# Optimization experiments

Measured on AMD Instinct MI355X. Metric: run time of the kernel, lower is better.

The kernel has to match this reference:

```python
import jax, jax.numpy as jnp
import numpy as np

N_WIRES = 4
N_LAYERS = 3
DIM = 2 ** N_WIRES  # 16-element statevector


def _ry(t):
    # RY(t) = [[cos(t/2), -sin(t/2)], [sin(t/2), cos(t/2)]]
    c, s = jnp.cos(t * 0.5), jnp.sin(t * 0.5)
    return jnp.stack([jnp.stack([c, -s], -1), jnp.stack([s, c], -1)], -2).astype(jnp.complex64)


def _rz(t):
    # RZ(t) = diag(e^{-it/2}, e^{+it/2})
    e = jnp.exp(-0.5j * t.astype(jnp.complex64))
    z = jnp.zeros_like(e)
    return jnp.stack([jnp.stack([e, z], -1), jnp.stack([z, jnp.conj(e)], -1)], -2)


def _rx(t):
    # RX(t) = [[cos(t/2), -i sin(t/2)], [-i sin(t/2), cos(t/2)]]
    c = jnp.cos(t * 0.5).astype(jnp.complex64)
    s = (-1j) * jnp.sin(t * 0.5).astype(jnp.complex64)
    return jnp.stack([jnp.stack([c, s], -1), jnp.stack([s, c], -1)], -2)


def _apply_1q(state, U, q):
    # state: (B, 16) complex; U: (B,2,2) batched or (2,2) shared; wire 0 = most significant
    B = state.shape[0]
    left, right = 2 ** q, 2 ** (N_WIRES - 1 - q)
    s = state.reshape(B, left, 2, right)
    if U.ndim == 3:
        s = jnp.einsum('bij,bajc->baic', U, s)
    else:
        s = jnp.einsum('ij,bajc->baic', U, s)
    return s.reshape(B, DIM)


def _apply_cnot(state, c):
    # CNOT with control wire c, target wire c+1 (adjacent)
    B = state.shape[0]
    left, right = 2 ** c, 2 ** (N_WIRES - 2 - c)
    s = state.reshape(B, left, 2, 2, right)
    s = s.at[:, :, 1].set(s[:, :, 1, ::-1])
    return s.reshape(B, DIM)


def setup_inputs() -> dict:
    key = jax.random.key(0)
    k1, k2 = jax.random.split(key)
    B = 524288
    x = jax.random.normal(k1, (B, N_WIRES), dtype=jnp.float32)
    params = jax.random.normal(k2, (N_LAYERS, N_WIRES, 3), dtype=jnp.float32) * 0.1
    return {'x': x, 'params': params}


def reference(x, params):
    B = x.shape[0]
    state = jnp.zeros((B, DIM), jnp.complex64).at[:, 0].set(1.0)
    # RYZXY encoding (batched gates)
    for i in range(N_WIRES):
        state = _apply_1q(state, _ry(x[:, i]), i)
        state = _apply_1q(state, _rz(x[:, (i + 1) % N_WIRES]), i)
        state = _apply_1q(state, _rx(x[:, (i + 2) % N_WIRES]), i)
        state = _apply_1q(state, _ry(x[:, (i + 3) % N_WIRES]), i)
    # variational layers: Rot(phi,theta,omega) = RZ(omega) @ RY(theta) @ RZ(phi), then CNOT chain
    for l in range(N_LAYERS):
        for q in range(N_WIRES):
            phi, th, om = params[l, q, 0], params[l, q, 1], params[l, q, 2]
            U = _rz(om) @ _ry(th) @ _rz(phi)
            state = _apply_1q(state, U, q)
        for q in range(N_WIRES - 1):
            state = _apply_cnot(state, q)
    # Pauli-Z expectation on each wire
    probs = (state.real ** 2 + state.imag ** 2).reshape((B,) + (2,) * N_WIRES)
    sign = jnp.array([1.0, -1.0], jnp.float32)
    outs = []
    for q in range(N_WIRES):
        shp = [1] * (N_WIRES + 1)
        shp[q + 1] = 2
        outs.append(jnp.sum(probs * sign.reshape(shp), axis=tuple(range(1, N_WIRES + 1))))
    return jnp.stack(outs, axis=1)  # (B, n_wires)
```

## Files before the change

### kernel.cpp

```cpp
#include <hip/hip_runtime.h>

#define N_WIRES 4
#define N_LAYERS 3
#define DIM 16

__device__ __forceinline__ float2 cmul(float2 a, float2 b) {
    return make_float2(a.x * b.x - a.y * b.y, a.x * b.y + a.y * b.x);
}
__device__ __forceinline__ float2 cadd(float2 a, float2 b) {
    return make_float2(a.x + b.x, a.y + b.y);
}

__global__ __launch_bounds__(256) void qenc_kernel(
    const float4* __restrict__ x4, const float* __restrict__ params,
    float4* __restrict__ out4, int B)
{
    __shared__ __align__(16) float Us[N_LAYERS * N_WIRES][8];
    const int t = threadIdx.x;
    if (t < N_LAYERS * N_WIRES) {
        const float phi = params[t * 3 + 0];
        const float th  = params[t * 3 + 1];
        const float om  = params[t * 3 + 2];
        float c, s, ca, sa, cb, sb;
        __sincosf(0.5f * th, &s, &c);
        __sincosf(0.5f * (phi + om), &sa, &ca);
        __sincosf(0.5f * (phi - om), &sb, &cb);
        Us[t][0] =  c * ca;  Us[t][1] = -c * sa;
        Us[t][2] = -s * cb;  Us[t][3] = -s * sb;
        Us[t][4] =  s * cb;  Us[t][5] = -s * sb;
        Us[t][6] =  c * ca;  Us[t][7] =  c * sa;
    }
    __syncthreads();

    const int b = blockIdx.x * blockDim.x + t;
    if (b >= B) return;

    const float4 xv = x4[b];
    const float xa[4] = {xv.x, xv.y, xv.z, xv.w};
    float cx[4], sx[4];
#pragma unroll
    for (int i = 0; i < 4; i++) __sincosf(0.5f * xa[i], &sx[i], &cx[i]);

    float2 w0[4], w1[4];
#pragma unroll
    for (int i = 0; i < 4; i++) {
        const int i1 = (i + 1) & 3, i2 = (i + 2) & 3, i3 = (i + 3) & 3;
        const float r0 = cx[i], r1 = sx[i];
        float2 n0 = make_float2(r0 * cx[i1], -r0 * sx[i1]);
        float2 n1 = make_float2(r1 * cx[i1],  r1 * sx[i1]);
        const float c2 = cx[i2], s2 = sx[i2];
        float2 m0 = make_float2(c2 * n0.x + s2 * n1.y,  c2 * n0.y - s2 * n1.x);
        float2 m1 = make_float2(s2 * n0.y + c2 * n1.x, -s2 * n0.x + c2 * n1.y);
        const float c3 = cx[i3], s3 = sx[i3];
        w0[i] = make_float2(c3 * m0.x - s3 * m1.x, c3 * m0.y - s3 * m1.y);
        w1[i] = make_float2(s3 * m0.x + c3 * m1.x, s3 * m0.y + c3 * m1.y);
    }

    float2 p01[4], p23[4];
    p01[0] = cmul(w0[0], w0[1]); p01[1] = cmul(w0[0], w1[1]);
    p01[2] = cmul(w1[0], w0[1]); p01[3] = cmul(w1[0], w1[1]);
    p23[0] = cmul(w0[2], w0[3]); p23[1] = cmul(w0[2], w1[3]);
    p23[2] = cmul(w1[2], w0[3]); p23[3] = cmul(w1[2], w1[3]);
    float2 st[16];
#pragma unroll
    for (int i = 0; i < 4; i++)
#pragma unroll
        for (int j = 0; j < 4; j++)
            st[i * 4 + j] = cmul(p01[i], p23[j]);

#pragma unroll
    for (int l = 0; l < N_LAYERS; l++) {
#pragma unroll
        for (int q = 0; q < N_WIRES; q++) {
            const float4* uv = (const float4*)Us[l * 4 + q];
            const float4 ua = uv[0], ub = uv[1];
            const float2 U00 = make_float2(ua.x, ua.y);
            const float2 U01 = make_float2(ua.z, ua.w);
            const float2 U10 = make_float2(ub.x, ub.y);
            const float2 U11 = make_float2(ub.z, ub.w);
            const int m = 8 >> q;
#pragma unroll
            for (int k = 0; k < 16; k++) {
                if (k & m) continue;
                const float2 v0 = st[k], v1 = st[k | m];
                st[k]     = cadd(cmul(U00, v0), cmul(U01, v1));
                st[k | m] = cadd(cmul(U10, v0), cmul(U11, v1));
            }
        }
#pragma unroll
        for (int c = 0; c < 3; c++) {
            const int cm = 8 >> c, tm = 4 >> c;
#pragma unroll
            for (int k = 0; k < 16; k++) {
                if ((k & cm) && !(k & tm)) {
                    const float2 tmp = st[k];
                    st[k] = st[k | tm];
                    st[k | tm] = tmp;
                }
            }
        }
    }

    float p[16];
#pragma unroll
    for (int k = 0; k < 16; k++) p[k] = st[k].x * st[k].x + st[k].y * st[k].y;

    float z[4];
#pragma unroll
    for (int q = 0; q < 4; q++) {
        const int m = 8 >> q;
        float acc = 0.f;
#pragma unroll
        for (int k = 0; k < 16; k++) acc += (k & m) ? -p[k] : p[k];
        z[q] = acc;
    }

    out4[b] = make_float4(z[0], z[1], z[2], z[3]);
}

extern "C" void kernel_launch(void* const* d_in, const int* in_sizes, int n_in,
                              void* d_out, int out_size, void* d_ws, size_t ws_size,
                              hipStream_t stream) {
    const float* x      = (const float*)d_in[0];
    const float* params = (const float*)d_in[1];
    float* out          = (float*)d_out;
    const int B = in_sizes[0] / 4;
    const int block = 256;
    const int grid = (B + block - 1) / block;
    qenc_kernel<<<grid, block, 0, stream>>>(
        (const float4*)x, params, (float4*)out, B);
}
```

Measured before the change: 86.81 us.

## Split gate-matrix setup into separate kernel and read unitaries from global workspace

The per-block shared-memory computation of the 12 Rot unitaries, and its __syncthreads barrier, is moved into a tiny setup kernel that writes them to workspace memory. The main kernel reads the coefficients as uniform scalar loads from global memory. The gate application and the final Z-expectation reduction are hand-unrolled with macros, and launch bounds now request 4 blocks per CU. The cost is a second kernel launch, and the compiler may now emit scalar global loads instead of LDS reads.

```diff
diff --git a/kernel.cpp b/kernel.cpp
--- a/kernel.cpp
+++ b/kernel.cpp
@@ -4,18 +4,7 @@
 #define N_LAYERS 3
 #define DIM 16
 
-__device__ __forceinline__ float2 cmul(float2 a, float2 b) {
-    return make_float2(a.x * b.x - a.y * b.y, a.x * b.y + a.y * b.x);
-}
-__device__ __forceinline__ float2 cadd(float2 a, float2 b) {
-    return make_float2(a.x + b.x, a.y + b.y);
-}
-
-__global__ __launch_bounds__(256) void qenc_kernel(
-    const float4* __restrict__ x4, const float* __restrict__ params,
-    float4* __restrict__ out4, int B)
-{
-    __shared__ __align__(16) float Us[N_LAYERS * N_WIRES][8];
+__global__ void qenc_setup(const float* __restrict__ params, float* __restrict__ W) {
     const int t = threadIdx.x;
     if (t < N_LAYERS * N_WIRES) {
         const float phi = params[t * 3 + 0];
@@ -25,14 +14,59 @@
         __sincosf(0.5f * th, &s, &c);
         __sincosf(0.5f * (phi + om), &sa, &ca);
         __sincosf(0.5f * (phi - om), &sb, &cb);
-        Us[t][0] =  c * ca;  Us[t][1] = -c * sa;
-        Us[t][2] = -s * cb;  Us[t][3] = -s * sb;
-        Us[t][4] =  s * cb;  Us[t][5] = -s * sb;
-        Us[t][6] =  c * ca;  Us[t][7] =  c * sa;
+        W[t * 8 + 0] =  c * ca;  W[t * 8 + 1] = -c * sa;
+        W[t * 8 + 2] = -s * cb;  W[t * 8 + 3] = -s * sb;
+        W[t * 8 + 4] =  s * cb;  W[t * 8 + 5] = -s * sb;
+        W[t * 8 + 6] =  c * ca;  W[t * 8 + 7] =  c * sa;
     }
-    __syncthreads();
+}
 
-    const int b = blockIdx.x * blockDim.x + t;
+__device__ __forceinline__ float2 cmul(float2 a, float2 b) {
+    return make_float2(a.x * b.x - a.y * b.y, a.x * b.y + a.y * b.x);
+}
+
+__device__ __forceinline__ void bfly(float2& A, float2& B,
+    float u00r, float u00i, float u01r, float u01i,
+    float u10r, float u10i, float u11r, float u11i) {
+    const float v0r = A.x, v0i = A.y, v1r = B.x, v1i = B.y;
+    A.x = u00r * v0r - u00i * v0i + u01r * v1r - u01i * v1i;
+    A.y = u00r * v0i + u00i * v0r + u01r * v1i + u01i * v1r;
+    B.x = u10r * v0r - u10i * v0i + u11r * v1r - u11i * v1i;
+    B.y = u10r * v0i + u10i * v0r + u11r * v1i + u11i * v1r;
+}
+
+#define GATE(g, a0,b0,a1,b1,a2,b2,a3,b3,a4,b4,a5,b5,a6,b6,a7,b7)              \
+    {                                                                          \
+        const float u00r = W[(g)*8+0], u00i = W[(g)*8+1];                      \
+        const float u01r = W[(g)*8+2], u01i = W[(g)*8+3];                      \
+        const float u10r = W[(g)*8+4], u10i = W[(g)*8+5];                      \
+        const float u11r = W[(g)*8+6], u11i = W[(g)*8+7];                      \
+        bfly(st[a0], st[b0], u00r,u00i,u01r,u01i,u10r,u10i,u11r,u11i);         \
+        bfly(st[a1], st[b1], u00r,u00i,u01r,u01i,u10r,u10i,u11r,u11i);         \
+        bfly(st[a2], st[b2], u00r,u00i,u01r,u01i,u10r,u10i,u11r,u11i);         \
+        bfly(st[a3], st[b3], u00r,u00i,u01r,u01i,u10r,u10i,u11r,u11i);         \
+        bfly(st[a4], st[b4], u00r,u00i,u01r,u01i,u10r,u10i,u11r,u11i);         \
+        bfly(st[a5], st[b5], u00r,u00i,u01r,u01i,u10r,u10i,u11r,u11i);         \
+        bfly(st[a6], st[b6], u00r,u00i,u01r,u01i,u10r,u10i,u11r,u11i);         \
+        bfly(st[a7], st[b7], u00r,u00i,u01r,u01i,u10r,u10i,u11r,u11i);         \
+    }
+
+#define SW(a,b) { const float2 t_ = st[a]; st[a] = st[b]; st[b] = t_; }
+
+#define LAYER(l)                                                               \
+    GATE((l)*4+0, 0,8, 1,9, 2,10, 3,11, 4,12, 5,13, 6,14, 7,15)                \
+    GATE((l)*4+1, 0,4, 1,5, 2,6,  3,7,  8,12, 9,13, 10,14, 11,15)              \
+    GATE((l)*4+2, 0,2, 1,3, 4,6,  5,7,  8,10, 9,11, 12,14, 13,15)              \
+    GATE((l)*4+3, 0,1, 2,3, 4,5,  6,7,  8,9,  10,11, 12,13, 14,15)             \
+     SW(8,12) SW(9,13) SW(10,14) SW(11,15)                      \
+     SW(4,6)  SW(5,7)  SW(12,14) SW(13,15)                      \
+     SW(2,3)  SW(6,7)  SW(10,11) SW(14,15)
+
+__global__ __launch_bounds__(256, 4) void qenc_main(
+    const float4* __restrict__ x4, const float* __restrict__ W,
+    float4* __restrict__ out4, int B)
+{
+    const int b = blockIdx.x * blockDim.x + threadIdx.x;
     if (b >= B) return;
 
     const float4 xv = x4[b];
@@ -61,61 +95,50 @@
     p01[2] = cmul(w1[0], w0[1]); p01[3] = cmul(w1[0], w1[1]);
     p23[0] = cmul(w0[2], w0[3]); p23[1] = cmul(w0[2], w1[3]);
     p23[2] = cmul(w1[2], w0[3]); p23[3] = cmul(w1[2], w1[3]);
+
     float2 st[16];
-#pragma unroll
-    for (int i = 0; i < 4; i++)
-#pragma unroll
-        for (int j = 0; j < 4; j++)
-            st[i * 4 + j] = cmul(p01[i], p23[j]);
+    st[ 0] = cmul(p01[0], p23[0]); st[ 1] = cmul(p01[0], p23[1]);
+    st[ 2] = cmul(p01[0], p23[2]); st[ 3] = cmul(p01[0], p23[3]);
+    st[ 4] = cmul(p01[1], p23[0]); st[ 5] = cmul(p01[1], p23[1]);
+    st[ 6] = cmul(p01[1], p23[2]); st[ 7] = cmul(p01[1], p23[3]);
+    st[ 8] = cmul(p01[2], p23[0]); st[ 9] = cmul(p01[2], p23[1]);
+    st[10] = cmul(p01[2], p23[2]); st[11] = cmul(p01[2], p23[3]);
+    st[12] = cmul(p01[3], p23[0]); st[13] = cmul(p01[3], p23[1]);
+    st[14] = cmul(p01[3], p23[2]); st[15] = cmul(p01[3], p23[3]);
 
-#pragma unroll
-    for (int l = 0; l < N_LAYERS; l++) {
-#pragma unroll
-        for (int q = 0; q < N_WIRES; q++) {
-            const float4* uv = (const float4*)Us[l * 4 + q];
-            const float4 ua = uv[0], ub = uv[1];
-            const float2 U00 = make_float2(ua.x, ua.y);
-            const float2 U01 = make_float2(ua.z, ua.w);
-            const float2 U10 = make_float2(ub.x, ub.y);
-            const float2 U11 = make_float2(ub.z, ub.w);
-            const int m = 8 >> q;
-#pragma unroll
-            for (int k = 0; k < 16; k++) {
-                if (k & m) continue;
-                const float2 v0 = st[k], v1 = st[k | m];
-                st[k]     = cadd(cmul(U00, v0), cmul(U01, v1));
-                st[k | m] = cadd(cmul(U10, v0), cmul(U11, v1));
-            }
-        }
-#pragma unroll
-        for (int c = 0; c < 3; c++) {
-            const int cm = 8 >> c, tm = 4 >> c;
-#pragma unroll
-            for (int k = 0; k < 16; k++) {
-                if ((k & cm) && !(k & tm)) {
-                    const float2 tmp = st[k];
-                    st[k] = st[k | tm];
-                    st[k | tm] = tmp;
-                }
-            }
-        }
-    }
+    LAYER(0)
+    LAYER(1)
+    LAYER(2)
 
-    float p[16];
-#pragma unroll
-    for (int k = 0; k < 16; k++) p[k] = st[k].x * st[k].x + st[k].y * st[k].y;
+    float q0  = st[ 0].x*st[ 0].x + st[ 0].y*st[ 0].y;
+    float q1  = st[ 1].x*st[ 1].x + st[ 1].y*st[ 1].y;
+    float q2  = st[ 2].x*st[ 2].x + st[ 2].y*st[ 2].y;
+    float q3  = st[ 3].x*st[ 3].x + st[ 3].y*st[ 3].y;
+    float q4  = st[ 4].x*st[ 4].x + st[ 4].y*st[ 4].y;
+    float q5  = st[ 5].x*st[ 5].x + st[ 5].y*st[ 5].y;
+    float q6  = st[ 6].x*st[ 6].x + st[ 6].y*st[ 6].y;
+    float q7  = st[ 7].x*st[ 7].x + st[ 7].y*st[ 7].y;
+    float q8  = st[ 8].x*st[ 8].x + st[ 8].y*st[ 8].y;
+    float q9  = st[ 9].x*st[ 9].x + st[ 9].y*st[ 9].y;
+    float q10 = st[10].x*st[10].x + st[10].y*st[10].y;
+    float q11 = st[11].x*st[11].x + st[11].y*st[11].y;
+    float q12 = st[12].x*st[12].x + st[12].y*st[12].y;
+    float q13 = st[13].x*st[13].x + st[13].y*st[13].y;
+    float q14 = st[14].x*st[14].x + st[14].y*st[14].y;
+    float q15 = st[15].x*st[15].x + st[15].y*st[15].y;
 
-    float z[4];
-#pragma unroll
-    for (int q = 0; q < 4; q++) {
-        const int m = 8 >> q;
-        float acc = 0.f;
-#pragma unroll
-        for (int k = 0; k < 16; k++) acc += (k & m) ? -p[k] : p[k];
-        z[q] = acc;
-    }
+    const float a0 = q0+q1,  a1 = q2+q3,  a2 = q4+q5,   a3 = q6+q7;
+    const float a4 = q8+q9,  a5 = q10+q11, a6 = q12+q13, a7 = q14+q15;
+    const float e0 = q0-q1,  e1 = q2-q3,  e2 = q4-q5,   e3 = q6-q7;
+    const float e4 = q8-q9,  e5 = q10-q11, e6 = q12-q13, e7 = q14-q15;
+    const float z3 = ((e0+e1)+(e2+e3)) + ((e4+e5)+(e6+e7));
+    const float b0 = a0+a1, b1 = a2+a3, b2 = a4+a5, b3 = a6+a7;
+    const float f0 = a0-a1, f1 = a2-a3, f2 = a4-a5, f3 = a6-a7;
+    const float z2 = (f0+f1) + (f2+f3);
+    const float z1 = (b0-b1) + (b2-b3);
+    const float z0 = (b0+b1) - (b2+b3);
 
-    out4[b] = make_float4(z[0], z[1], z[2], z[3]);
+    out4[b] = make_float4(z0, z1, z2, z3);
 }
 
 extern "C" void kernel_launch(void* const* d_in, const int* in_sizes, int n_in,
@@ -124,9 +147,12 @@
     const float* x      = (const float*)d_in[0];
     const float* params = (const float*)d_in[1];
     float* out          = (float*)d_out;
+    float* W            = (float*)d_ws;
     const int B = in_sizes[0] / 4;
+
+    qenc_setup<<<1, 64, 0, stream>>>(params, W);
+
     const int block = 256;
     const int grid = (B + block - 1) / block;
-    qenc_kernel<<<grid, block, 0, stream>>>(
-        (const float4*)x, params, (float4*)out, B);
+    qenc_main<<<grid, block, 0, stream>>>((const float4*)x, W, (float4*)out, B);
 }
```

After: 89.50 us. +3.1%, slower.
